# Optimization experiments

Measured on AMD Instinct MI355X. Metric: run time of the kernel, lower is better.

Reference implementation:

```python
import jax, jax.numpy as jnp
import numpy as np

B, S, D, H = 4, 2048, 1024, 16
HD = D // H  # 64


def setup_inputs() -> dict:
    key = jax.random.key(0)
    ks = jax.random.split(key, 16)
    inv = 1.0 / np.sqrt(D)
    inv_hd = 1.0 / np.sqrt(D)
    inp = {
        "query": jax.random.normal(ks[0], (B, S, D), jnp.float32),
        "key": jax.random.normal(ks[1], (B, S, D), jnp.float32),
        "value": jax.random.normal(ks[2], (B, S, D), jnp.float32),
        # causal mask: True entries are masked out (masked_fill semantics)
        "mask": jnp.triu(jnp.ones((S, S), jnp.bool_), k=1),
        # weights stored [in, out] (math identical to torch x @ W.T)
        "Wq": jax.random.normal(ks[3], (D, D), jnp.float32) * inv,
        "Wk": jax.random.normal(ks[4], (D, D), jnp.float32) * inv,
        "Wv": jax.random.normal(ks[5], (D, D), jnp.float32) * inv,
        "wq_h": jax.random.normal(ks[6], (D, HD), jnp.float32) * inv_hd,
        "bq_h": jax.random.normal(ks[7], (HD,), jnp.float32) * inv_hd,
        "wk_h": jax.random.normal(ks[8], (D, HD), jnp.float32) * inv_hd,
        "bk_h": jax.random.normal(ks[9], (HD,), jnp.float32) * inv_hd,
        "wv_h": jax.random.normal(ks[10], (D, HD), jnp.float32) * inv_hd,
        "bv_h": jax.random.normal(ks[11], (HD,), jnp.float32) * inv_hd,
        "Wo": jax.random.normal(ks[12], (D, D), jnp.float32) * inv,
    }
    return inp


def reference(query, key, value, mask, Wq, Wk, Wv, wq_h, bq_h, wk_h, bk_h, wv_h, bv_h, Wo):
    # full-width projections
    q = jnp.einsum('bsd,de->bse', query, Wq)
    k = jnp.einsum('bsd,de->bse', key, Wk)
    v = jnp.einsum('bsd,de->bse', value, Wv)
    # per-head projections: the torch loop reuses the SAME weights every
    # iteration, so all H head outputs are identical -> compute once.
    qh = jnp.einsum('bsd,dh->bsh', q, wq_h) + bq_h  # [B,S,HD]
    kh = jnp.einsum('bsd,dh->bsh', k, wk_h) + bk_h
    vh = jnp.einsum('bsd,dh->bsh', v, wv_h) + bv_h
    scores = jnp.einsum('bsh,bth->bst', qh, kh) / jnp.sqrt(jnp.float32(HD))
    scores = jnp.where(mask, jnp.float32(-1e9), scores)
    attn = jax.nn.softmax(scores, axis=-1)
    out_h = jnp.einsum('bst,bth->bsh', attn, vh)  # [B,S,HD]
    out = jnp.tile(out_h, (1, 1, H))  # cat of H identical heads -> [B,S,D]
    # final linear; dropout is identity at inference
    return jnp.einsum('bsd,de->bse', out, Wo)
```

## Files before the change

### kernel.cpp

```cpp
#include <hip/hip_runtime.h>
#include <math.h>

#define S_LEN 2048
#define BATCH 4
#define DMODEL 1024
#define HDIM 64
#define NROWS (BATCH * S_LEN)

typedef __attribute__((ext_vector_type(8))) short bf16x8;
typedef __attribute__((ext_vector_type(4))) float f32x4;

__device__ inline ushort f2bf(float f) {
    union { float f; uint u; } v{f};
    uint r = v.u + 0x7fffu + ((v.u >> 16) & 1u);
    return (ushort)(r >> 16);
}

__global__ __launch_bounds__(256) void prep_weff_mfma(
    const float* __restrict__ A0, const float* __restrict__ A1, const float* __restrict__ A2,
    const float* __restrict__ B0, const float* __restrict__ B1, const float* __restrict__ B2,
    ushort* __restrict__ T0, ushort* __restrict__ T1, ushort* __restrict__ T2)
{
    const int z = blockIdx.y;
    const float* A = (z == 0) ? A0 : (z == 1) ? A1 : A2;
    const float* B = (z == 0) ? B0 : (z == 1) ? B1 : B2;
    ushort* T      = (z == 0) ? T0 : (z == 1) ? T1 : T2;

    __shared__ ushort As[64][72];
    __shared__ ushort Bt[64][72];

    const int t    = threadIdx.x;
    const int w    = t >> 6;
    const int lane = t & 63;
    const int lg   = lane >> 4;
    const int lc   = lane & 15;
    const int r0   = blockIdx.x * 64;

    f32x4 acc[4] = {};

    for (int k0 = 0; k0 < 1024; k0 += 64) {
        __syncthreads();
        #pragma unroll
        for (int q = 0; q < 4; ++q) {
            int u   = t * 4 + q;
            int row = u >> 4;
            int c4  = (u & 15) << 2;
            float4 v = *reinterpret_cast<const float4*>(
                A + (size_t)(r0 + row) * 1024 + k0 + c4);
            ushort4 p;
            p.x = f2bf(v.x); p.y = f2bf(v.y); p.z = f2bf(v.z); p.w = f2bf(v.w);
            *reinterpret_cast<ushort4*>(&As[row][c4]) = p;
        }
        #pragma unroll
        for (int q = 0; q < 4; ++q) {
            int u  = t * 4 + q;
            int kr = u >> 4;
            int h4 = (u & 15) << 2;
            float4 v = *reinterpret_cast<const float4*>(
                B + (size_t)(k0 + kr) * 64 + h4);
            Bt[h4 + 0][kr] = f2bf(v.x);
            Bt[h4 + 1][kr] = f2bf(v.y);
            Bt[h4 + 2][kr] = f2bf(v.z);
            Bt[h4 + 3][kr] = f2bf(v.w);
        }
        __syncthreads();

        bf16x8 af0 = *reinterpret_cast<const bf16x8*>(&As[16 * w + lc][lg * 8]);
        bf16x8 af1 = *reinterpret_cast<const bf16x8*>(&As[16 * w + lc][32 + lg * 8]);
        #pragma unroll
        for (int n = 0; n < 4; ++n) {
            bf16x8 bf0 = *reinterpret_cast<const bf16x8*>(&Bt[16 * n + lc][lg * 8]);
            bf16x8 bf1 = *reinterpret_cast<const bf16x8*>(&Bt[16 * n + lc][32 + lg * 8]);
            acc[n] = __builtin_amdgcn_mfma_f32_16x16x32_bf16(af0, bf0, acc[n], 0, 0, 0);
            acc[n] = __builtin_amdgcn_mfma_f32_16x16x32_bf16(af1, bf1, acc[n], 0, 0, 0);
        }
    }

    #pragma unroll
    for (int n = 0; n < 4; ++n)
        #pragma unroll
        for (int reg = 0; reg < 4; ++reg)
            T[(size_t)(16 * n + lc) * 1024 + r0 + 16 * w + 4 * lg + reg] =
                f2bf(acc[n][reg]);
}

__global__ __launch_bounds__(256) void fold_wo(const float* __restrict__ Wo,
                                               ushort* __restrict__ WoT)
{
    int idx = blockIdx.x * 256 + threadIdx.x;
    int j = idx >> 10;
    int e = idx & 1023;
    float s = 0.f;
    #pragma unroll
    for (int h = 0; h < 16; ++h)
        s += Wo[(size_t)((h << 6) + j) * 1024 + e];
    WoT[(size_t)e * 64 + j] = f2bf(s);
}

__global__ __launch_bounds__(256) void proj_mfma(
    const float* __restrict__ A0, const float* __restrict__ A1, const float* __restrict__ A2,
    const ushort* __restrict__ W0, const ushort* __restrict__ W1, const ushort* __restrict__ W2,
    const float* __restrict__ b0, const float* __restrict__ b1, const float* __restrict__ b2,
    ushort* __restrict__ O0, ushort* __restrict__ O1, ushort* __restrict__ O2)
{
    const int z = blockIdx.y;
    const float* A  = (z == 0) ? A0 : (z == 1) ? A1 : A2;
    const ushort* W = (z == 0) ? W0 : (z == 1) ? W1 : W2;
    const float* bias = (z == 0) ? b0 : (z == 1) ? b1 : b2;
    ushort* O       = (z == 0) ? O0 : (z == 1) ? O1 : O2;

    __shared__ ushort As[64][72];
    __shared__ ushort Bs[64][72];

    const int t    = threadIdx.x;
    const int w    = t >> 6;
    const int lane = t & 63;
    const int lg   = lane >> 4;
    const int lc   = lane & 15;
    const int r0   = blockIdx.x * 64;

    f32x4 acc[4] = {};

    for (int k0 = 0; k0 < 1024; k0 += 64) {
        __syncthreads();
        #pragma unroll
        for (int q = 0; q < 4; ++q) {
            int u   = t * 4 + q;
            int row = u >> 4;
            int c4  = (u & 15) << 2;
            float4 v = *reinterpret_cast<const float4*>(
                A + (size_t)(r0 + row) * 1024 + k0 + c4);
            ushort4 p;
            p.x = f2bf(v.x); p.y = f2bf(v.y); p.z = f2bf(v.z); p.w = f2bf(v.w);
            *reinterpret_cast<ushort4*>(&As[row][c4]) = p;
        }
        #pragma unroll
        for (int q = 0; q < 2; ++q) {
            int u   = t * 2 + q;
            int row = u >> 3;
            int c8  = (u & 7) << 3;
            uint4 v = *reinterpret_cast<const uint4*>(W + (size_t)row * 1024 + k0 + c8);
            *reinterpret_cast<uint4*>(&Bs[row][c8]) = v;
        }
        __syncthreads();

        bf16x8 af0 = *reinterpret_cast<const bf16x8*>(&As[16 * w + lc][lg * 8]);
        bf16x8 af1 = *reinterpret_cast<const bf16x8*>(&As[16 * w + lc][32 + lg * 8]);
        #pragma unroll
        for (int n = 0; n < 4; ++n) {
            bf16x8 bf0 = *reinterpret_cast<const bf16x8*>(&Bs[16 * n + lc][lg * 8]);
            bf16x8 bf1 = *reinterpret_cast<const bf16x8*>(&Bs[16 * n + lc][32 + lg * 8]);
            acc[n] = __builtin_amdgcn_mfma_f32_16x16x32_bf16(af0, bf0, acc[n], 0, 0, 0);
            acc[n] = __builtin_amdgcn_mfma_f32_16x16x32_bf16(af1, bf1, acc[n], 0, 0, 0);
        }
    }

    #pragma unroll
    for (int n = 0; n < 4; ++n) {
        float bv = bias[16 * n + lc];
        #pragma unroll
        for (int reg = 0; reg < 4; ++reg) {
            int row = r0 + 16 * w + 4 * lg + reg;
            O[(size_t)row * 64 + 16 * n + lc] = f2bf(acc[n][reg] + bv);
        }
    }
}

__global__ __launch_bounds__(256) void transpose_v(const ushort* __restrict__ vh,
                                                   ushort* __restrict__ vhT)
{
    const int b  = blockIdx.y;
    const int r0 = blockIdx.x * 64;
    __shared__ ushort T[64][72];
    const int t = threadIdx.x;

    #pragma unroll
    for (int q = 0; q < 2; ++q) {
        int u  = t * 2 + q;
        int s  = u >> 3;
        int d8 = (u & 7) << 3;
        uint4 v = *reinterpret_cast<const uint4*>(
            vh + ((size_t)b * S_LEN + r0 + s) * 64 + d8);
        *reinterpret_cast<uint4*>(&T[s][d8]) = v;
    }
    __syncthreads();
    #pragma unroll
    for (int q = 0; q < 2; ++q) {
        int u  = t * 2 + q;
        int d  = u >> 3;
        int s8 = (u & 7) << 3;
        uint4 o;
        uint* ow = reinterpret_cast<uint*>(&o);
        #pragma unroll
        for (int i = 0; i < 4; ++i)
            ow[i] = (uint)T[s8 + 2 * i][d] | ((uint)T[s8 + 2 * i + 1][d] << 16);
        *reinterpret_cast<uint4*>(
            vhT + (size_t)b * 64 * S_LEN + (size_t)d * S_LEN + r0 + s8) = o;
    }
}

__global__ __launch_bounds__(256) void flash_mfma(
    const ushort* __restrict__ qh, const ushort* __restrict__ kh,
    const ushort* __restrict__ vhT,
    float* __restrict__ Opart, float* __restrict__ mpart, float* __restrict__ lpart)
{
    const int b = blockIdx.y;
    const int u = blockIdx.x;
    int gi = 0;
    #pragma unroll
    for (int gg = 0; gg < 7; ++gg)
        if (u >= 2 * (gg + 1) * (gg + 2)) gi = gg + 1;
    const int rem = u - 2 * gi * (gi + 1);
    const int dq  = rem / (gi + 1);
    const int c   = rem - dq * (gi + 1);
    const int qt  = 4 * gi + dq;
    const int r0  = qt * 64;
    const int kvbase = c << 8;
    const int slot = b * 144 + u;

    __shared__ ushort Qs[64][72];
    __shared__ ushort Ks[64][72];
    __shared__ ushort Vt[64][72];
    __shared__ ushort Pw[4][16][72];

    const int t    = threadIdx.x;
    const int w    = t >> 6;
    const int lane = t & 63;
    const int lg   = lane >> 4;
    const int lc   = lane & 15;

    const ushort* qb  = qh  + (size_t)b * S_LEN * 64;
    const ushort* kb  = kh  + (size_t)b * S_LEN * 64;
    const ushort* vtb = vhT + (size_t)b * 64 * S_LEN;

    #pragma unroll
    for (int q = 0; q < 2; ++q) {
        int uu  = t * 2 + q;
        int row = uu >> 3;
        int c8  = (uu & 7) << 3;
        *reinterpret_cast<uint4*>(&Qs[row][c8]) =
            *reinterpret_cast<const uint4*>(qb + (size_t)(r0 + row) * 64 + c8);
    }
    __syncthreads();
    bf16x8 qf0 = *reinterpret_cast<const bf16x8*>(&Qs[16 * w + lc][lg * 8]);
    bf16x8 qf1 = *reinterpret_cast<const bf16x8*>(&Qs[16 * w + lc][32 + lg * 8]);

    f32x4 od[4] = {};
    float m = -INFINITY, lsum = 0.f;
    const int qrow = r0 + 16 * w + lc;

    const int ntt = min(4, ((r0 + 63 - kvbase) >> 6) + 1);
    for (int tt = 0; tt < ntt; ++tt) {
        const int t0 = kvbase + (tt << 6);
        __syncthreads();
        #pragma unroll
        for (int q = 0; q < 2; ++q) {
            int uu  = t * 2 + q;
            int row = uu >> 3;
            int c8  = (uu & 7) << 3;
            *reinterpret_cast<uint4*>(&Ks[row][c8]) =
                *reinterpret_cast<const uint4*>(kb + (size_t)(t0 + row) * 64 + c8);
            *reinterpret_cast<uint4*>(&Vt[row][c8]) =
                *reinterpret_cast<const uint4*>(vtb + (size_t)row * S_LEN + t0 + c8);
        }
        __syncthreads();

        if (t0 <= r0 + 16 * w + 15) {
            f32x4 s[4] = {};
            #pragma unroll
            for (int a = 0; a < 4; ++a) {
                bf16x8 kf0 = *reinterpret_cast<const bf16x8*>(&Ks[16 * a + lc][lg * 8]);
                bf16x8 kf1 = *reinterpret_cast<const bf16x8*>(&Ks[16 * a + lc][32 + lg * 8]);
                s[a] = __builtin_amdgcn_mfma_f32_16x16x32_bf16(kf0, qf0, s[a], 0, 0, 0);
                s[a] = __builtin_amdgcn_mfma_f32_16x16x32_bf16(kf1, qf1, s[a], 0, 0, 0);
            }
            float rm = -1e30f;
            #pragma unroll
            for (int a = 0; a < 4; ++a)
                #pragma unroll
                for (int reg = 0; reg < 4; ++reg) {
                    int kv = t0 + 16 * a + 4 * lg + reg;
                    float v = s[a][reg] * 0.125f;
                    if (kv > qrow) v = -1e30f;
                    s[a][reg] = v;
                    rm = fmaxf(rm, v);
                }
            rm = fmaxf(rm, __shfl_xor(rm, 16));
            rm = fmaxf(rm, __shfl_xor(rm, 32));
            float mn = fmaxf(m, rm);
            float sc = __expf(m - mn);
            float rs = 0.f;
            #pragma unroll
            for (int a = 0; a < 4; ++a)
                #pragma unroll
                for (int reg = 0; reg < 4; ++reg) {
                    float p = __expf(s[a][reg] - mn);
                    s[a][reg] = p;
                    rs += p;
                }
            rs += __shfl_xor(rs, 16);
            rs += __shfl_xor(rs, 32);
            lsum = lsum * sc + rs;
            m = mn;
            #pragma unroll
            for (int di = 0; di < 4; ++di) od[di] *= sc;

            #pragma unroll
            for (int a = 0; a < 4; ++a)
                #pragma unroll
                for (int rp = 0; rp < 2; ++rp) {
                    uint pk = (uint)f2bf(s[a][2 * rp]) |
                              ((uint)f2bf(s[a][2 * rp + 1]) << 16);
                    *reinterpret_cast<uint*>(&Pw[w][lc][16 * a + 4 * lg + 2 * rp]) = pk;
                }
            bf16x8 pf0 = *reinterpret_cast<const bf16x8*>(&Pw[w][lc][lg * 8]);
            bf16x8 pf1 = *reinterpret_cast<const bf16x8*>(&Pw[w][lc][32 + lg * 8]);
            #pragma unroll
            for (int di = 0; di < 4; ++di) {
                bf16x8 vf0 = *reinterpret_cast<const bf16x8*>(&Vt[16 * di + lc][lg * 8]);
                bf16x8 vf1 = *reinterpret_cast<const bf16x8*>(&Vt[16 * di + lc][32 + lg * 8]);
                od[di] = __builtin_amdgcn_mfma_f32_16x16x32_bf16(vf0, pf0, od[di], 0, 0, 0);
                od[di] = __builtin_amdgcn_mfma_f32_16x16x32_bf16(vf1, pf1, od[di], 0, 0, 0);
            }
        }
    }

    #pragma unroll
    for (int di = 0; di < 4; ++di)
        #pragma unroll
        for (int reg = 0; reg < 4; ++reg)
            Opart[(size_t)slot * 4096 + (16 * di + 4 * lg + reg) * 64 + 16 * w + lc] =
                od[di][reg];
    if (lg == 0) {
        mpart[slot * 64 + 16 * w + lc] = m;
        lpart[slot * 64 + 16 * w + lc] = lsum;
    }
}

__global__ __launch_bounds__(256) void flash_combine(
    const float* __restrict__ Opart, const float* __restrict__ mpart,
    const float* __restrict__ lpart, ushort* __restrict__ oh)
{
    const int qt = blockIdx.x, b = blockIdx.y;
    const int gi = qt >> 2;
    const int nc = gi + 1;
    const int ubase = 2 * gi * (gi + 1) + (qt & 3) * (gi + 1);
    __shared__ float T[64][65];

    const int t  = threadIdx.x;
    const int q  = t & 63;
    const int d0 = (t >> 6) << 4;

    float mc[8];
    float M = -INFINITY;
    #pragma unroll
    for (int cc = 0; cc < 8; ++cc) {
        mc[cc] = (cc < nc) ? mpart[(b * 144 + ubase + cc) * 64 + q] : -INFINITY;
        M = fmaxf(M, mc[cc]);
    }
    float L = 0.f;
    float acc[16] = {};
    for (int cc = 0; cc < nc; ++cc) {
        const int slot = b * 144 + ubase + cc;
        float wgt = __expf(mc[cc] - M);
        L += lpart[slot * 64 + q] * wgt;
        const float* op = Opart + (size_t)slot * 4096 + q;
        #pragma unroll
        for (int i = 0; i < 16; ++i)
            acc[i] += wgt * op[(d0 + i) * 64];
    }
    float inv = 1.f / L;
    #pragma unroll
    for (int i = 0; i < 16; ++i) T[q][d0 + i] = acc[i] * inv;
    __syncthreads();

    const int q2 = t >> 2;
    const int ds = (t & 3) << 4;
    uint wbuf[8];
    #pragma unroll
    for (int i = 0; i < 8; ++i)
        wbuf[i] = (uint)f2bf(T[q2][ds + 2 * i]) |
                  ((uint)f2bf(T[q2][ds + 2 * i + 1]) << 16);
    ushort* dst = oh + ((size_t)b * S_LEN + qt * 64 + q2) * 64 + ds;
    uint4 o1, o2;
    o1.x = wbuf[0]; o1.y = wbuf[1]; o1.z = wbuf[2]; o1.w = wbuf[3];
    o2.x = wbuf[4]; o2.y = wbuf[5]; o2.z = wbuf[6]; o2.w = wbuf[7];
    *reinterpret_cast<uint4*>(dst)     = o1;
    *reinterpret_cast<uint4*>(dst + 8) = o2;
}

__global__ __launch_bounds__(256) void epilogue_mfma(
    const ushort* __restrict__ oh, const ushort* __restrict__ WoT,
    float* __restrict__ out)
{
    const int r0 = blockIdx.x * 64;
    const int c0 = blockIdx.y * 128;
    __shared__ ushort As[64][72];
    __shared__ ushort Bs[128][72];

    const int t    = threadIdx.x;
    const int w    = t >> 6;
    const int lane = t & 63;
    const int lg   = lane >> 4;
    const int lc   = lane & 15;

    #pragma unroll
    for (int q = 0; q < 2; ++q) {
        int u   = t * 2 + q;
        int row = u >> 3;
        int c8  = (u & 7) << 3;
        *reinterpret_cast<uint4*>(&As[row][c8]) =
            *reinterpret_cast<const uint4*>(oh + (size_t)(r0 + row) * 64 + c8);
    }
    #pragma unroll
    for (int q = 0; q < 4; ++q) {
        int u   = t * 4 + q;
        int row = u >> 3;
        int c8  = (u & 7) << 3;
        *reinterpret_cast<uint4*>(&Bs[row][c8]) =
            *reinterpret_cast<const uint4*>(WoT + (size_t)(c0 + row) * 64 + c8);
    }
    __syncthreads();

    bf16x8 af0 = *reinterpret_cast<const bf16x8*>(&As[16 * w + lc][lg * 8]);
    bf16x8 af1 = *reinterpret_cast<const bf16x8*>(&As[16 * w + lc][32 + lg * 8]);
    f32x4 acc[8] = {};
    #pragma unroll
    for (int n = 0; n < 8; ++n) {
        bf16x8 bf0 = *reinterpret_cast<const bf16x8*>(&Bs[16 * n + lc][lg * 8]);
        bf16x8 bf1 = *reinterpret_cast<const bf16x8*>(&Bs[16 * n + lc][32 + lg * 8]);
        acc[n] = __builtin_amdgcn_mfma_f32_16x16x32_bf16(af0, bf0, acc[n], 0, 0, 0);
        acc[n] = __builtin_amdgcn_mfma_f32_16x16x32_bf16(af1, bf1, acc[n], 0, 0, 0);
    }
    #pragma unroll
    for (int n = 0; n < 8; ++n)
        #pragma unroll
        for (int reg = 0; reg < 4; ++reg)
            out[(size_t)(r0 + 16 * w + 4 * lg + reg) * 1024 + c0 + 16 * n + lc] =
                acc[n][reg];
}

extern "C" void kernel_launch(void* const* d_in, const int* in_sizes, int n_in,
                              void* d_out, int out_size, void* d_ws, size_t ws_size,
                              hipStream_t stream)
{
    const float* query = (const float*)d_in[0];
    const float* key   = (const float*)d_in[1];
    const float* value = (const float*)d_in[2];
    const float* Wq   = (const float*)d_in[4];
    const float* Wk   = (const float*)d_in[5];
    const float* Wv   = (const float*)d_in[6];
    const float* wq_h = (const float*)d_in[7];
    const float* bq_h = (const float*)d_in[8];
    const float* wk_h = (const float*)d_in[9];
    const float* bk_h = (const float*)d_in[10];
    const float* wv_h = (const float*)d_in[11];
    const float* bv_h = (const float*)d_in[12];
    const float* Wo   = (const float*)d_in[13];
    float* out = (float*)d_out;

    ushort* W16  = (ushort*)d_ws;
    ushort* WT0  = W16;
    ushort* WT1  = W16 + 65536;
    ushort* WT2  = W16 + 131072;
    ushort* WoT  = W16 + 196608;
    ushort* qh   = W16 + 262144;
    ushort* kh   = qh + 524288;
    ushort* vh   = kh + 524288;
    ushort* vhT  = vh + 524288;
    ushort* oh   = vhT + 524288;

    float* Opart = out;
    float* mpart = out + 2359296;
    float* lpart = out + 2396160;

    prep_weff_mfma<<<dim3(16, 3), 256, 0, stream>>>(
        Wq, Wk, Wv, wq_h, wk_h, wv_h, WT0, WT1, WT2);
    fold_wo<<<256, 256, 0, stream>>>(Wo, WoT);

    proj_mfma<<<dim3(NROWS / 64, 3), 256, 0, stream>>>(
        query, key, value, WT0, WT1, WT2, bq_h, bk_h, bv_h, qh, kh, vh);

    transpose_v<<<dim3(S_LEN / 64, BATCH), 256, 0, stream>>>(vh, vhT);

    flash_mfma<<<dim3(144, BATCH), 256, 0, stream>>>(
        qh, kh, vhT, Opart, mpart, lpart);
    flash_combine<<<dim3(S_LEN / 64, BATCH), 256, 0, stream>>>(
        Opart, mpart, lpart, oh);

    epilogue_mfma<<<dim3(NROWS / 64, DMODEL / 128), 256, 0, stream>>>(oh, WoT, out);
}
```

Baseline: 83.42 us.

## Split-K the projection GEMM with register prefetch and a separate reduce kernel

The projection kernel now splits the K dimension into two halves, which doubles the grid from 384 to 768 blocks, and writes fp32 partial sums to a workspace. A new reduce kernel adds the two partials and the bias, then converts the result to bf16. The main loop also prefetches the next global tile into registers while the current tile is being computed. This trades more blocks and better latency hiding for extra fp32 partial traffic and one more kernel launch.

```diff
diff --git a/kernel.cpp b/kernel.cpp
--- a/kernel.cpp
+++ b/kernel.cpp
@@ -97,17 +97,14 @@
     WoT[(size_t)e * 64 + j] = f2bf(s);
 }
 
-__global__ __launch_bounds__(256) void proj_mfma(
+__global__ __launch_bounds__(256) void proj_mfma_sk(
     const float* __restrict__ A0, const float* __restrict__ A1, const float* __restrict__ A2,
     const ushort* __restrict__ W0, const ushort* __restrict__ W1, const ushort* __restrict__ W2,
-    const float* __restrict__ b0, const float* __restrict__ b1, const float* __restrict__ b2,
-    ushort* __restrict__ O0, ushort* __restrict__ O1, ushort* __restrict__ O2)
+    float* __restrict__ P)
 {
     const int z = blockIdx.y;
     const float* A  = (z == 0) ? A0 : (z == 1) ? A1 : A2;
     const ushort* W = (z == 0) ? W0 : (z == 1) ? W1 : W2;
-    const float* bias = (z == 0) ? b0 : (z == 1) ? b1 : b2;
-    ushort* O       = (z == 0) ? O0 : (z == 1) ? O1 : O2;
 
     __shared__ ushort As[64][72];
     __shared__ ushort Bs[64][72];
@@ -117,32 +114,59 @@
     const int lane = t & 63;
     const int lg   = lane >> 4;
     const int lc   = lane & 15;
-    const int r0   = blockIdx.x * 64;
+    const int rt   = blockIdx.x >> 1;
+    const int kh2  = blockIdx.x & 1;
+    const int r0   = rt * 64;
+    const int kbase = kh2 << 9;
+
+    const int ar = (t * 4) >> 4;
 
     f32x4 acc[4] = {};
-
-    for (int k0 = 0; k0 < 1024; k0 += 64) {
-        __syncthreads();
+    float4 aL[4];
+    uint4  wL[2];
+
+    auto issue = [&](int k0) {
         #pragma unroll
         for (int q = 0; q < 4; ++q) {
             int u   = t * 4 + q;
             int row = u >> 4;
             int c4  = (u & 15) << 2;
-            float4 v = *reinterpret_cast<const float4*>(
+            aL[q] = *reinterpret_cast<const float4*>(
                 A + (size_t)(r0 + row) * 1024 + k0 + c4);
-            ushort4 p;
-            p.x = f2bf(v.x); p.y = f2bf(v.y); p.z = f2bf(v.z); p.w = f2bf(v.w);
-            *reinterpret_cast<ushort4*>(&As[row][c4]) = p;
         }
         #pragma unroll
         for (int q = 0; q < 2; ++q) {
             int u   = t * 2 + q;
             int row = u >> 3;
             int c8  = (u & 7) << 3;
-            uint4 v = *reinterpret_cast<const uint4*>(W + (size_t)row * 1024 + k0 + c8);
-            *reinterpret_cast<uint4*>(&Bs[row][c8]) = v;
-        }
+            wL[q] = *reinterpret_cast<const uint4*>(W + (size_t)row * 1024 + k0 + c8);
+        }
+    };
+
+    issue(kbase);
+
+    for (int it = 0; it < 8; ++it) {
+        const int k0 = kbase + (it << 6);
         __syncthreads();
+        #pragma unroll
+        for (int q = 0; q < 4; ++q) {
+            int u   = t * 4 + q;
+            int row = u >> 4;
+            int c4  = (u & 15) << 2;
+            ushort4 p;
+            p.x = f2bf(aL[q].x); p.y = f2bf(aL[q].y);
+            p.z = f2bf(aL[q].z); p.w = f2bf(aL[q].w);
+            *reinterpret_cast<ushort4*>(&As[row][c4]) = p;
+        }
+        #pragma unroll
+        for (int q = 0; q < 2; ++q) {
+            int u   = t * 2 + q;
+            int row = u >> 3;
+            int c8  = (u & 7) << 3;
+            *reinterpret_cast<uint4*>(&Bs[row][c8]) = wL[q];
+        }
+        __syncthreads();
+        if (it < 7) issue(k0 + 64);
 
         bf16x8 af0 = *reinterpret_cast<const bf16x8*>(&As[16 * w + lc][lg * 8]);
         bf16x8 af1 = *reinterpret_cast<const bf16x8*>(&As[16 * w + lc][32 + lg * 8]);
@@ -155,15 +179,39 @@
         }
     }
 
-    #pragma unroll
-    for (int n = 0; n < 4; ++n) {
-        float bv = bias[16 * n + lc];
-        #pragma unroll
-        for (int reg = 0; reg < 4; ++reg) {
-            int row = r0 + 16 * w + 4 * lg + reg;
-            O[(size_t)row * 64 + 16 * n + lc] = f2bf(acc[n][reg] + bv);
-        }
-    }
+    float* Pz = P + (((size_t)z * 2 + kh2) * NROWS) * 64;
+    #pragma unroll
+    for (int n = 0; n < 4; ++n)
+        #pragma unroll
+        for (int reg = 0; reg < 4; ++reg)
+            Pz[(size_t)(r0 + 16 * w + 4 * lg + reg) * 64 + 16 * n + lc] =
+                acc[n][reg];
+}
+
+__global__ __launch_bounds__(256) void proj_reduce(
+    const float* __restrict__ P,
+    const float* __restrict__ b0, const float* __restrict__ b1, const float* __restrict__ b2,
+    ushort* __restrict__ O0, ushort* __restrict__ O1, ushort* __restrict__ O2)
+{
+    int idx = blockIdx.x * 256 + threadIdx.x;
+    int z   = idx >> 17;
+    int g   = idx & 131071;
+    int row = g >> 4;
+    int n4  = (g & 15) << 2;
+    const float* bias = (z == 0) ? b0 : (z == 1) ? b1 : b2;
+    ushort* O         = (z == 0) ? O0 : (z == 1) ? O1 : O2;
+
+    const float* p0 = P + (((size_t)z * 2 + 0) * NROWS + row) * 64 + n4;
+    const float* p1 = P + (((size_t)z * 2 + 1) * NROWS + row) * 64 + n4;
+    float4 a = *reinterpret_cast<const float4*>(p0);
+    float4 c = *reinterpret_cast<const float4*>(p1);
+    float4 bb = *reinterpret_cast<const float4*>(bias + n4);
+    ushort4 o;
+    o.x = f2bf(a.x + c.x + bb.x);
+    o.y = f2bf(a.y + c.y + bb.y);
+    o.z = f2bf(a.z + c.z + bb.z);
+    o.w = f2bf(a.w + c.w + bb.w);
+    *reinterpret_cast<ushort4*>(O + (size_t)row * 64 + n4) = o;
 }
 
 __global__ __launch_bounds__(256) void transpose_v(const ushort* __restrict__ vh,
@@ -469,6 +517,7 @@
     ushort* vh   = kh + 524288;
     ushort* vhT  = vh + 524288;
     ushort* oh   = vhT + 524288;
+    float*  Ppart = (float*)(W16 + 2883584);
 
     float* Opart = out;
     float* mpart = out + 2359296;
@@ -478,8 +527,10 @@
         Wq, Wk, Wv, wq_h, wk_h, wv_h, WT0, WT1, WT2);
     fold_wo<<<256, 256, 0, stream>>>(Wo, WoT);
 
-    proj_mfma<<<dim3(NROWS / 64, 3), 256, 0, stream>>>(
-        query, key, value, WT0, WT1, WT2, bq_h, bk_h, bv_h, qh, kh, vh);
+    proj_mfma_sk<<<dim3(256, 3), 256, 0, stream>>>(
+        query, key, value, WT0, WT1, WT2, Ppart);
+    proj_reduce<<<1536, 256, 0, stream>>>(
+        Ppart, bq_h, bk_h, bv_h, qh, kh, vh);
 
     transpose_v<<<dim3(S_LEN / 64, BATCH), 256, 0, stream>>>(vh, vhT);
 
```

New measurement: 90.90 us. +9.0%, slower.

## Use split-K register-direct MFMA GEMMs for weight folding and projections

Applied to the files above, without the earlier changes.

Replaces the shared-memory tiled projection and weight-fold GEMMs with kernels that load bf16 fragments straight from global memory into registers. These kernels use 16-row tiles and split K across the four waves, then reduce the partial sums through shared memory. A new small kernel pre-transposes the per-head weights to bf16 so the fold GEMM can use the same direct-load scheme. The intent is more blocks, better occupancy and prefetched loads without per-K-step barriers. In exchange it adds an extra launch and a shared-memory reduction, and the uncoalesced-looking strided global loads may waste bandwidth.

```diff
diff --git a/kernel.cpp b/kernel.cpp
--- a/kernel.cpp
+++ b/kernel.cpp
@@ -16,154 +16,212 @@
     return (ushort)(r >> 16);
 }
 
-__global__ __launch_bounds__(256) void prep_weff_mfma(
-    const float* __restrict__ A0, const float* __restrict__ A1, const float* __restrict__ A2,
+__device__ inline bf16x8 cvt8(float4 a, float4 b) {
+    bf16x8 r;
+    r[0] = (short)f2bf(a.x); r[1] = (short)f2bf(a.y);
+    r[2] = (short)f2bf(a.z); r[3] = (short)f2bf(a.w);
+    r[4] = (short)f2bf(b.x); r[5] = (short)f2bf(b.y);
+    r[6] = (short)f2bf(b.z); r[7] = (short)f2bf(b.w);
+    return r;
+}
+
+__global__ __launch_bounds__(256) void transpose_wh(
     const float* __restrict__ B0, const float* __restrict__ B1, const float* __restrict__ B2,
     ushort* __restrict__ T0, ushort* __restrict__ T1, ushort* __restrict__ T2)
 {
     const int z = blockIdx.y;
-    const float* A = (z == 0) ? A0 : (z == 1) ? A1 : A2;
     const float* B = (z == 0) ? B0 : (z == 1) ? B1 : B2;
     ushort* T      = (z == 0) ? T0 : (z == 1) ? T1 : T2;
-
-    __shared__ ushort As[64][72];
-    __shared__ ushort Bt[64][72];
+    const int kr0 = blockIdx.x * 64;
+    __shared__ ushort Ts[64][72];
+    const int t = threadIdx.x;
+
+    #pragma unroll
+    for (int q = 0; q < 4; ++q) {
+        int u   = t * 4 + q;
+        int row = u >> 4;
+        int c4  = (u & 15) << 2;
+        float4 v = *reinterpret_cast<const float4*>(
+            B + (size_t)(kr0 + row) * 64 + c4);
+        Ts[row][c4 + 0] = f2bf(v.x); Ts[row][c4 + 1] = f2bf(v.y);
+        Ts[row][c4 + 2] = f2bf(v.z); Ts[row][c4 + 3] = f2bf(v.w);
+    }
+    __syncthreads();
+    #pragma unroll
+    for (int q = 0; q < 2; ++q) {
+        int u  = t * 2 + q;
+        int h  = u >> 3;
+        int k8 = (u & 7) << 3;
+        uint4 o;
+        uint* ow = reinterpret_cast<uint*>(&o);
+        #pragma unroll
+        for (int i = 0; i < 4; ++i)
+            ow[i] = (uint)Ts[k8 + 2 * i][h] | ((uint)Ts[k8 + 2 * i + 1][h] << 16);
+        *reinterpret_cast<uint4*>(T + (size_t)h * 1024 + kr0 + k8) = o;
+    }
+}
+
+__global__ __launch_bounds__(256, 6) void prep_direct(
+    const float* __restrict__ A0, const float* __restrict__ A1, const float* __restrict__ A2,
+    const ushort* __restrict__ W0, const ushort* __restrict__ W1, const ushort* __restrict__ W2,
+    ushort* __restrict__ T0, ushort* __restrict__ T1, ushort* __restrict__ T2)
+{
+    const int z = blockIdx.y;
+    const float* A  = (z == 0) ? A0 : (z == 1) ? A1 : A2;
+    const ushort* W = (z == 0) ? W0 : (z == 1) ? W1 : W2;
+    ushort* T       = (z == 0) ? T0 : (z == 1) ? T1 : T2;
+
+    __shared__ float Pr[4][16][64];
 
     const int t    = threadIdx.x;
     const int w    = t >> 6;
     const int lane = t & 63;
     const int lg   = lane >> 4;
     const int lc   = lane & 15;
-    const int r0   = blockIdx.x * 64;
+    const int r0   = blockIdx.x * 16;
+
+    const float*  Ap = A + (size_t)(r0 + lc) * 1024 + (w << 8) + (lg << 3);
+    const ushort* Bp = W + (size_t)lc * 1024 + (w << 8) + (lg << 3);
 
     f32x4 acc[4] = {};
-
-    for (int k0 = 0; k0 < 1024; k0 += 64) {
-        __syncthreads();
-        #pragma unroll
-        for (int q = 0; q < 4; ++q) {
-            int u   = t * 4 + q;
-            int row = u >> 4;
-            int c4  = (u & 15) << 2;
-            float4 v = *reinterpret_cast<const float4*>(
-                A + (size_t)(r0 + row) * 1024 + k0 + c4);
-            ushort4 p;
-            p.x = f2bf(v.x); p.y = f2bf(v.y); p.z = f2bf(v.z); p.w = f2bf(v.w);
-            *reinterpret_cast<ushort4*>(&As[row][c4]) = p;
+    float4 a0[2], a1[2];
+    uint4  bl[2][4];
+
+    #pragma unroll
+    for (int d = 0; d < 2; ++d) {
+        a0[d] = *reinterpret_cast<const float4*>(Ap + d * 32);
+        a1[d] = *reinterpret_cast<const float4*>(Ap + d * 32 + 4);
+        #pragma unroll
+        for (int n = 0; n < 4; ++n)
+            bl[d][n] = *reinterpret_cast<const uint4*>(Bp + n * 16384 + d * 32);
+    }
+
+    #pragma unroll
+    for (int ks = 0; ks < 8; ++ks) {
+        const int d = ks & 1;
+        bf16x8 af = cvt8(a0[d], a1[d]);
+        bf16x8 bfr[4];
+        #pragma unroll
+        for (int n = 0; n < 4; ++n)
+            bfr[n] = __builtin_bit_cast(bf16x8, bl[d][n]);
+        if (ks < 6) {
+            a0[d] = *reinterpret_cast<const float4*>(Ap + (ks + 2) * 32);
+            a1[d] = *reinterpret_cast<const float4*>(Ap + (ks + 2) * 32 + 4);
+            #pragma unroll
+            for (int n = 0; n < 4; ++n)
+                bl[d][n] = *reinterpret_cast<const uint4*>(Bp + n * 16384 + (ks + 2) * 32);
         }
         #pragma unroll
-        for (int q = 0; q < 4; ++q) {
-            int u  = t * 4 + q;
-            int kr = u >> 4;
-            int h4 = (u & 15) << 2;
-            float4 v = *reinterpret_cast<const float4*>(
-                B + (size_t)(k0 + kr) * 64 + h4);
-            Bt[h4 + 0][kr] = f2bf(v.x);
-            Bt[h4 + 1][kr] = f2bf(v.y);
-            Bt[h4 + 2][kr] = f2bf(v.z);
-            Bt[h4 + 3][kr] = f2bf(v.w);
-        }
-        __syncthreads();
-
-        bf16x8 af0 = *reinterpret_cast<const bf16x8*>(&As[16 * w + lc][lg * 8]);
-        bf16x8 af1 = *reinterpret_cast<const bf16x8*>(&As[16 * w + lc][32 + lg * 8]);
-        #pragma unroll
-        for (int n = 0; n < 4; ++n) {
-            bf16x8 bf0 = *reinterpret_cast<const bf16x8*>(&Bt[16 * n + lc][lg * 8]);
-            bf16x8 bf1 = *reinterpret_cast<const bf16x8*>(&Bt[16 * n + lc][32 + lg * 8]);
-            acc[n] = __builtin_amdgcn_mfma_f32_16x16x32_bf16(af0, bf0, acc[n], 0, 0, 0);
-            acc[n] = __builtin_amdgcn_mfma_f32_16x16x32_bf16(af1, bf1, acc[n], 0, 0, 0);
-        }
+        for (int n = 0; n < 4; ++n)
+            acc[n] = __builtin_amdgcn_mfma_f32_16x16x32_bf16(af, bfr[n], acc[n], 0, 0, 0);
     }
 
     #pragma unroll
     for (int n = 0; n < 4; ++n)
         #pragma unroll
         for (int reg = 0; reg < 4; ++reg)
-            T[(size_t)(16 * n + lc) * 1024 + r0 + 16 * w + 4 * lg + reg] =
-                f2bf(acc[n][reg]);
-}
-
-__global__ __launch_bounds__(256) void fold_wo(const float* __restrict__ Wo,
-                                               ushort* __restrict__ WoT)
-{
-    int idx = blockIdx.x * 256 + threadIdx.x;
-    int j = idx >> 10;
-    int e = idx & 1023;
-    float s = 0.f;
-    #pragma unroll
-    for (int h = 0; h < 16; ++h)
-        s += Wo[(size_t)((h << 6) + j) * 1024 + e];
-    WoT[(size_t)e * 64 + j] = f2bf(s);
-}
-
-__global__ __launch_bounds__(256) void proj_mfma(
+            Pr[w][4 * lg + reg][16 * n + lc] = acc[n][reg];
+    __syncthreads();
+
+    const int row = t >> 4;
+    const int col = (t & 15) << 2;
+    float s[4];
+    #pragma unroll
+    for (int i = 0; i < 4; ++i)
+        s[i] = Pr[0][row][col + i] + Pr[1][row][col + i] +
+               Pr[2][row][col + i] + Pr[3][row][col + i];
+    #pragma unroll
+    for (int i = 0; i < 4; ++i)
+        T[(size_t)(col + i) * 1024 + r0 + row] = f2bf(s[i]);
+}
+
+__global__ __launch_bounds__(256, 6) void proj_direct(
     const float* __restrict__ A0, const float* __restrict__ A1, const float* __restrict__ A2,
     const ushort* __restrict__ W0, const ushort* __restrict__ W1, const ushort* __restrict__ W2,
     const float* __restrict__ b0, const float* __restrict__ b1, const float* __restrict__ b2,
     ushort* __restrict__ O0, ushort* __restrict__ O1, ushort* __restrict__ O2)
 {
     const int z = blockIdx.y;
-    const float* A  = (z == 0) ? A0 : (z == 1) ? A1 : A2;
-    const ushort* W = (z == 0) ? W0 : (z == 1) ? W1 : W2;
+    const float* A    = (z == 0) ? A0 : (z == 1) ? A1 : A2;
+    const ushort* W   = (z == 0) ? W0 : (z == 1) ? W1 : W2;
     const float* bias = (z == 0) ? b0 : (z == 1) ? b1 : b2;
-    ushort* O       = (z == 0) ? O0 : (z == 1) ? O1 : O2;
-
-    __shared__ ushort As[64][72];
-    __shared__ ushort Bs[64][72];
+    ushort* O         = (z == 0) ? O0 : (z == 1) ? O1 : O2;
+
+    __shared__ float Pr[4][16][64];
 
     const int t    = threadIdx.x;
     const int w    = t >> 6;
     const int lane = t & 63;
     const int lg   = lane >> 4;
     const int lc   = lane & 15;
-    const int r0   = blockIdx.x * 64;
+    const int r0   = blockIdx.x * 16;
+
+    const float*  Ap = A + (size_t)(r0 + lc) * 1024 + (w << 8) + (lg << 3);
+    const ushort* Bp = W + (size_t)lc * 1024 + (w << 8) + (lg << 3);
 
     f32x4 acc[4] = {};
-
-    for (int k0 = 0; k0 < 1024; k0 += 64) {
-        __syncthreads();
-        #pragma unroll
-        for (int q = 0; q < 4; ++q) {
-            int u   = t * 4 + q;
-            int row = u >> 4;
-            int c4  = (u & 15) << 2;
-            float4 v = *reinterpret_cast<const float4*>(
-                A + (size_t)(r0 + row) * 1024 + k0 + c4);
-            ushort4 p;
-            p.x = f2bf(v.x); p.y = f2bf(v.y); p.z = f2bf(v.z); p.w = f2bf(v.w);
-            *reinterpret_cast<ushort4*>(&As[row][c4]) = p;
+    float4 a0[2], a1[2];
+    uint4  bl[2][4];
+
+    #pragma unroll
+    for (int d = 0; d < 2; ++d) {
+        a0[d] = *reinterpret_cast<const float4*>(Ap + d * 32);
+        a1[d] = *reinterpret_cast<const float4*>(Ap + d * 32 + 4);
+        #pragma unroll
+        for (int n = 0; n < 4; ++n)
+            bl[d][n] = *reinterpret_cast<const uint4*>(Bp + n * 16384 + d * 32);
+    }
+
+    #pragma unroll
+    for (int ks = 0; ks < 8; ++ks) {
+        const int d = ks & 1;
+        bf16x8 af = cvt8(a0[d], a1[d]);
+        bf16x8 bfr[4];
+        #pragma unroll
+        for (int n = 0; n < 4; ++n)
+            bfr[n] = __builtin_bit_cast(bf16x8, bl[d][n]);
+        if (ks < 6) {
+            a0[d] = *reinterpret_cast<const float4*>(Ap + (ks + 2) * 32);
+            a1[d] = *reinterpret_cast<const float4*>(Ap + (ks + 2) * 32 + 4);
+            #pragma unroll
+            for (int n = 0; n < 4; ++n)
+                bl[d][n] = *reinterpret_cast<const uint4*>(Bp + n * 16384 + (ks + 2) * 32);
         }
         #pragma unroll
-        for (int q = 0; q < 2; ++q) {
-            int u   = t * 2 + q;
-            int row = u >> 3;
-            int c8  = (u & 7) << 3;
-            uint4 v = *reinterpret_cast<const uint4*>(W + (size_t)row * 1024 + k0 + c8);
-            *reinterpret_cast<uint4*>(&Bs[row][c8]) = v;
-        }
-        __syncthreads();
-
-        bf16x8 af0 = *reinterpret_cast<const bf16x8*>(&As[16 * w + lc][lg * 8]);
-        bf16x8 af1 = *reinterpret_cast<const bf16x8*>(&As[16 * w + lc][32 + lg * 8]);
-        #pragma unroll
-        for (int n = 0; n < 4; ++n) {
-            bf16x8 bf0 = *reinterpret_cast<const bf16x8*>(&Bs[16 * n + lc][lg * 8]);
-            bf16x8 bf1 = *reinterpret_cast<const bf16x8*>(&Bs[16 * n + lc][32 + lg * 8]);
-            acc[n] = __builtin_amdgcn_mfma_f32_16x16x32_bf16(af0, bf0, acc[n], 0, 0, 0);
-            acc[n] = __builtin_amdgcn_mfma_f32_16x16x32_bf16(af1, bf1, acc[n], 0, 0, 0);
-        }
-    }
-
-    #pragma unroll
-    for (int n = 0; n < 4; ++n) {
-        float bv = bias[16 * n + lc];
-        #pragma unroll
-        for (int reg = 0; reg < 4; ++reg) {
-            int row = r0 + 16 * w + 4 * lg + reg;
-            O[(size_t)row * 64 + 16 * n + lc] = f2bf(acc[n][reg] + bv);
-        }
-    }
+        for (int n = 0; n < 4; ++n)
+            acc[n] = __builtin_amdgcn_mfma_f32_16x16x32_bf16(af, bfr[n], acc[n], 0, 0, 0);
+    }
+
+    #pragma unroll
+    for (int n = 0; n < 4; ++n)
+        #pragma unroll
+        for (int reg = 0; reg < 4; ++reg)
+            Pr[w][4 * lg + reg][16 * n + lc] = acc[n][reg];
+    __syncthreads();
+
+    const int row = t >> 4;
+    const int col = (t & 15) << 2;
+    float4 bb = *reinterpret_cast<const float4*>(bias + col);
+    float s0 = Pr[0][row][col + 0] + Pr[1][row][col + 0] + Pr[2][row][col + 0] + Pr[3][row][col + 0] + bb.x;
+    float s1 = Pr[0][row][col + 1] + Pr[1][row][col + 1] + Pr[2][row][col + 1] + Pr[3][row][col + 1] + bb.y;
+    float s2 = Pr[0][row][col + 2] + Pr[1][row][col + 2] + Pr[2][row][col + 2] + Pr[3][row][col + 2] + bb.z;
+    float s3 = Pr[0][row][col + 3] + Pr[1][row][col + 3] + Pr[2][row][col + 3] + Pr[3][row][col + 3] + bb.w;
+    ushort4 o;
+    o.x = f2bf(s0); o.y = f2bf(s1); o.z = f2bf(s2); o.w = f2bf(s3);
+    *reinterpret_cast<ushort4*>(O + (size_t)(r0 + row) * 64 + col) = o;
+}
+
+__global__ __launch_bounds__(256) void fold_wo(const float* __restrict__ Wo,
+                                               ushort* __restrict__ WoT)
+{
+    int idx = blockIdx.x * 256 + threadIdx.x;
+    int j = idx >> 10;
+    int e = idx & 1023;
+    float s = 0.f;
+    #pragma unroll
+    for (int h = 0; h < 16; ++h)
+        s += Wo[(size_t)((h << 6) + j) * 1024 + e];
+    WoT[(size_t)e * 64 + j] = f2bf(s);
 }
 
 __global__ __launch_bounds__(256) void transpose_v(const ushort* __restrict__ vh,
@@ -469,16 +527,22 @@
     ushort* vh   = kh + 524288;
     ushort* vhT  = vh + 524288;
     ushort* oh   = vhT + 524288;
+    ushort* whT0 = oh + 524288;
+    ushort* whT1 = whT0 + 65536;
+    ushort* whT2 = whT1 + 65536;
 
     float* Opart = out;
     float* mpart = out + 2359296;
     float* lpart = out + 2396160;
 
-    prep_weff_mfma<<<dim3(16, 3), 256, 0, stream>>>(
-        Wq, Wk, Wv, wq_h, wk_h, wv_h, WT0, WT1, WT2);
+    transpose_wh<<<dim3(16, 3), 256, 0, stream>>>(
+        wq_h, wk_h, wv_h, whT0, whT1, whT2);
     fold_wo<<<256, 256, 0, stream>>>(Wo, WoT);
 
-    proj_mfma<<<dim3(NROWS / 64, 3), 256, 0, stream>>>(
+    prep_direct<<<dim3(64, 3), 256, 0, stream>>>(
+        Wq, Wk, Wv, whT0, whT1, whT2, WT0, WT1, WT2);
+
+    proj_direct<<<dim3(512, 3), 256, 0, stream>>>(
         query, key, value, WT0, WT1, WT2, bq_h, bk_h, bv_h, qh, kh, vh);
 
     transpose_v<<<dim3(S_LEN / 64, BATCH), 256, 0, stream>>>(vh, vhT);
```

Measured after the change: 84.20 us. About the same (+0.9%).
